# Kernel tuning notes

Hardware: AMD Instinct MI355X
Metric: run time of the kernel (lower is better)

The kernel has to match this reference:

```python
import jax, jax.numpy as jnp
import numpy as np

NEG_SLOPE = 0.2  # PyG GATConv default leaky_relu slope
EPS = 1e-16      # PyG softmax denominator epsilon


def gat_conv(x, src, dst, W, a_src, a_dst, num_nodes):
    """Single-head PyG GATConv (concat=True, heads=1, no bias), self-loops already in src/dst."""
    h = x @ W                                  # [N, out]
    alpha_src = h @ a_src                      # [N]
    alpha_dst = h @ a_dst                      # [N]
    e = jax.nn.leaky_relu(alpha_src[src] + alpha_dst[dst], NEG_SLOPE)  # [E]
    # segment softmax over destination nodes
    m = jax.ops.segment_max(e, dst, num_segments=num_nodes)           # [N]
    ex = jnp.exp(e - m[dst])                                          # [E]
    denom = jax.ops.segment_sum(ex, dst, num_segments=num_nodes)      # [N]
    alpha = ex / (denom[dst] + EPS)                                   # [E]
    # scatter-add weighted source features to destinations
    out = jax.ops.segment_sum(h[src] * alpha[:, None], dst, num_segments=num_nodes)
    return out


def setup_inputs() -> dict:
    key = jax.random.key(0)
    N, E, F_in, H, C = 100000, 1600000, 256, 64, 40
    ks = jax.random.split(key, 12)
    x = jax.random.normal(ks[0], (N, F_in), dtype=jnp.float32)
    edge_index = jax.random.randint(ks[1], (2, E), 0, N, dtype=jnp.int64)
    s = 0.1
    return {
        "x": x,
        "edge_index": edge_index,
        "W0": jax.random.normal(ks[2], (F_in, H), dtype=jnp.float32) * s,
        "asrc0": jax.random.normal(ks[3], (H,), dtype=jnp.float32) * s,
        "adst0": jax.random.normal(ks[4], (H,), dtype=jnp.float32) * s,
        "W1": jax.random.normal(ks[5], (H, H), dtype=jnp.float32) * s,
        "asrc1": jax.random.normal(ks[6], (H,), dtype=jnp.float32) * s,
        "adst1": jax.random.normal(ks[7], (H,), dtype=jnp.float32) * s,
        "W2": jax.random.normal(ks[8], (H, C), dtype=jnp.float32) * s,
        "asrc2": jax.random.normal(ks[9], (C,), dtype=jnp.float32) * s,
        "adst2": jax.random.normal(ks[10], (C,), dtype=jnp.float32) * s,
    }


def reference(x, edge_index, W0, asrc0, adst0, W1, asrc1, adst1, W2, asrc2, adst2):
    N = x.shape[0]
    # PyG GATConv add_self_loops=True: append (i, i) for every node
    loops = jnp.arange(N, dtype=edge_index.dtype)
    src = jnp.concatenate([edge_index[0], loops])
    dst = jnp.concatenate([edge_index[1], loops])
    params = [(W0, asrc0, adst0), (W1, asrc1, adst1), (W2, asrc2, adst2)]
    h = x
    for i, (W, a_s, a_d) in enumerate(params):
        h = gat_conv(h, src, dst, W, a_s, a_d, N)
        # type_norm='None' -> batch_norm is identity; eval mode -> no dropout/side losses
        if i != len(params) - 1:
            h = jax.nn.relu(h)
    return h
```

## Files before the change

### kernel.cpp

```cpp
#include <hip/hip_runtime.h>
#include <hip/hip_fp16.h>

#define CAP 56
#define BINW 128
#define CAPB 2560
#define CHUNK 4096
#define NEG_SLOPE 0.2f

__global__ void k_initcur(int* __restrict__ gcur, int nbin) {
    int i = blockIdx.x * blockDim.x + threadIdx.x;
    if (i < nbin) gcur[i] = i * CAPB;
}

__global__ __launch_bounds__(256) void k_bin(const int* __restrict__ esrc,
                                             const int* __restrict__ edst,
                                             int E, int N, int nbin,
                                             int* __restrict__ gcur,
                                             int* __restrict__ binbuf) {
    __shared__ int hist[1024];
    __shared__ int base[1024];

    const int tid = threadIdx.x;
    const int tot = E + N;
    const int start = blockIdx.x * CHUNK;
    const int end = (start + CHUNK < tot) ? start + CHUNK : tot;

    for (int i = tid; i < nbin; i += 256) hist[i] = 0;
    __syncthreads();

    for (int i = start + tid; i < end; i += 256) {
        int d = (i < E) ? edst[i] : (i - E);
        atomicAdd(&hist[d >> 7], 1);
    }
    __syncthreads();

    for (int i = tid; i < nbin; i += 256) {
        int h = hist[i];
        base[i] = h ? atomicAdd(&gcur[i], h) : 0;
    }
    __syncthreads();
    for (int i = tid; i < nbin; i += 256) hist[i] = 0;
    __syncthreads();

    for (int i = start + tid; i < end; i += 256) {
        int s, d;
        if (i < E) { s = esrc[i]; d = edst[i]; }
        else       { s = i - E;   d = s; }
        int b = d >> 7;
        int p = base[b] + atomicAdd(&hist[b], 1);
        if (p < (b + 1) * CAPB)
            binbuf[p] = ((d & (BINW - 1)) << 17) | s;
    }
}

__global__ __launch_bounds__(256) void k_bucket_bin(const int* __restrict__ binbuf,
                                                    const int* __restrict__ gcur,
                                                    int N,
                                                    int* __restrict__ cnt,
                                                    int* __restrict__ bucket) {
    __shared__ int lcnt[BINW];
    __shared__ int lb[BINW * CAP];

    const int tid = threadIdx.x;
    const int b = blockIdx.x;

    int n = gcur[b] - b * CAPB;
    if (n > CAPB) n = CAPB;

    for (int i = tid; i < BINW; i += 256) lcnt[i] = 0;
    for (int i = tid; i < BINW * CAP; i += 256) lb[i] = 0;
    __syncthreads();

    const int* src = binbuf + (size_t)b * CAPB;
    for (int i = tid; i < n; i += 256) {
        int x = src[i];
        int s = x & 0x1ffff;
        int dl = x >> 17;
        int p = atomicAdd(&lcnt[dl], 1);
        if (p < CAP) lb[dl * CAP + p] = s;
    }
    __syncthreads();

    size_t gbase = (size_t)b * BINW * CAP;
    for (int i = tid; i < BINW * CAP; i += 256)
        bucket[gbase + i] = lb[i];
    for (int i = tid; i < BINW; i += 256) {
        int v = b * BINW + i;
        if (v < N) cnt[v] = (lcnt[i] < CAP) ? lcnt[i] : CAP;
    }
}

template <int K, int FR>
__global__ __launch_bounds__(256) void k_gemm_tiled(const float* __restrict__ X,
                                                    const float* __restrict__ W,
                                                    const float* __restrict__ a_s,
                                                    const float* __restrict__ a_d,
                                                    __half* __restrict__ H16,
                                                    float* __restrict__ AS,
                                                    float* __restrict__ AD,
                                                    int N) {
    constexpr int BM = 128, BK = 32;
    constexpr int FP = 64;
    constexpr int XS = BK + 4;

    __shared__ float Xs[BM * XS];
    __shared__ float Ws[BK * FP];

    const int tid = threadIdx.x;
    const int tx = tid & 15, ty = tid >> 4;
    const int row0 = blockIdx.x * BM;

    float acc[8][4];
#pragma unroll
    for (int i = 0; i < 8; ++i)
#pragma unroll
        for (int j = 0; j < 4; ++j) acc[i][j] = 0.f;

    for (int k0 = 0; k0 < K; k0 += BK) {
#pragma unroll
        for (int i = 0; i < 4; ++i) {
            int idx = tid + 256 * i;
            int r = idx >> 3;
            int c4 = idx & 7;
            int gr = row0 + r;
            float4 v = make_float4(0.f, 0.f, 0.f, 0.f);
            if (gr < N) v = *reinterpret_cast<const float4*>(X + (size_t)gr * K + k0 + c4 * 4);
            *reinterpret_cast<float4*>(&Xs[r * XS + c4 * 4]) = v;
        }
        for (int i = tid; i < BK * FP; i += 256) {
            int r = i >> 6, c = i & 63;
            Ws[i] = (c < FR) ? W[(size_t)(k0 + r) * FR + c] : 0.f;
        }
        __syncthreads();

#pragma unroll
        for (int kq = 0; kq < BK; kq += 4) {
            float4 av[8];
#pragma unroll
            for (int i = 0; i < 8; ++i)
                av[i] = *reinterpret_cast<const float4*>(&Xs[(ty + (i << 4)) * XS + kq]);
#pragma unroll
            for (int kk = 0; kk < 4; ++kk) {
                float4 bwv = *reinterpret_cast<const float4*>(&Ws[(kq + kk) * FP + 4 * tx]);
#pragma unroll
                for (int i = 0; i < 8; ++i) {
                    float xs = (kk == 0) ? av[i].x : (kk == 1) ? av[i].y : (kk == 2) ? av[i].z : av[i].w;
                    acc[i][0] = fmaf(xs, bwv.x, acc[i][0]);
                    acc[i][1] = fmaf(xs, bwv.y, acc[i][1]);
                    acc[i][2] = fmaf(xs, bwv.z, acc[i][2]);
                    acc[i][3] = fmaf(xs, bwv.w, acc[i][3]);
                }
            }
        }
        __syncthreads();
    }

    float asv[4], adv[4];
#pragma unroll
    for (int j = 0; j < 4; ++j) {
        int col = 4 * tx + j;
        asv[j] = (col < FR) ? a_s[col] : 0.f;
        adv[j] = (col < FR) ? a_d[col] : 0.f;
    }

#pragma unroll
    for (int i = 0; i < 8; ++i) {
        int gr = row0 + ty + 16 * i;
        float rs = 0.f, rd = 0.f;
#pragma unroll
        for (int j = 0; j < 4; ++j) {
            rs = fmaf(acc[i][j], asv[j], rs);
            rd = fmaf(acc[i][j], adv[j], rd);
        }
#pragma unroll
        for (int off = 1; off < 16; off <<= 1) {
            rs += __shfl_xor(rs, off);
            rd += __shfl_xor(rd, off);
        }
        if (gr < N) {
            if (4 * tx < FR) {
                __half2 p0 = __floats2half2_rn(acc[i][0], acc[i][1]);
                __half2 p1 = __floats2half2_rn(acc[i][2], acc[i][3]);
                uint2 pk;
                pk.x = *reinterpret_cast<unsigned*>(&p0);
                pk.y = *reinterpret_cast<unsigned*>(&p1);
                *reinterpret_cast<uint2*>(&H16[(size_t)gr * FR + 4 * tx]) = pk;
            }
            if (tx == 0) { AS[gr] = rs; AD[gr] = rd; }
        }
    }
}

template <int F, bool RELU>
__global__ __launch_bounds__(256) void k_aggregate(const __half* __restrict__ H16,
                                                   const float* __restrict__ AS,
                                                   const float* __restrict__ AD,
                                                   const int* __restrict__ cnt,
                                                   const int* __restrict__ bucket,
                                                   float* __restrict__ OUT,
                                                   int N) {
    int wid  = (blockIdx.x * blockDim.x + threadIdx.x) >> 6;
    int lane = threadIdx.x & 63;
    if (wid >= N) return;
    int v = wid;

    int deg = cnt[v];

    int s = -1;
    if (lane < deg) s = bucket[(size_t)v * CAP + lane];

    float adv = AD[v];
    float ev  = -3.4e38f;
    if (s >= 0) {
        float t = AS[s] + adv;
        ev = (t > 0.f) ? t : NEG_SLOPE * t;
    }

    float m = ev;
#pragma unroll
    for (int off = 32; off; off >>= 1) m = fmaxf(m, __shfl_xor(m, off));

    float ex = (s >= 0) ? __expf(ev - m) : 0.f;

    float dsum = ex;
#pragma unroll
    for (int off = 32; off; off >>= 1) dsum += __shfl_xor(dsum, off);

    float inv = 1.f / (dsum + 1e-16f);

    float acc0 = 0.f, acc1 = 0.f, acc2 = 0.f, acc3 = 0.f;
    int e = 0;
    for (; e + 4 <= deg; e += 4) {
        int   s0 = __shfl(s, e),      s1 = __shfl(s, e + 1);
        int   s2 = __shfl(s, e + 2),  s3 = __shfl(s, e + 3);
        float a0 = __shfl(ex, e),     a1 = __shfl(ex, e + 1);
        float a2 = __shfl(ex, e + 2), a3 = __shfl(ex, e + 3);
        if (lane < F) {
            float h0 = __half2float(H16[(size_t)s0 * F + lane]);
            float h1 = __half2float(H16[(size_t)s1 * F + lane]);
            float h2 = __half2float(H16[(size_t)s2 * F + lane]);
            float h3 = __half2float(H16[(size_t)s3 * F + lane]);
            acc0 = fmaf(h0, a0, acc0);
            acc1 = fmaf(h1, a1, acc1);
            acc2 = fmaf(h2, a2, acc2);
            acc3 = fmaf(h3, a3, acc3);
        }
    }
    for (; e < deg; ++e) {
        int   se = __shfl(s, e);
        float al = __shfl(ex, e);
        if (lane < F) acc0 = fmaf(__half2float(H16[(size_t)se * F + lane]), al, acc0);
    }
    float acc = (acc0 + acc1) + (acc2 + acc3);
    acc *= inv;
    if (RELU) acc = fmaxf(acc, 0.f);
    if (lane < F) OUT[(size_t)v * F + lane] = acc;
}

extern "C" void kernel_launch(void* const* d_in, const int* in_sizes, int n_in,
                              void* d_out, int out_size, void* d_ws, size_t ws_size,
                              hipStream_t stream) {
    const float* x     = (const float*)d_in[0];
    const int*   ei    = (const int*)d_in[1];
    const float* W0    = (const float*)d_in[2];
    const float* asrc0 = (const float*)d_in[3];
    const float* adst0 = (const float*)d_in[4];
    const float* W1    = (const float*)d_in[5];
    const float* asrc1 = (const float*)d_in[6];
    const float* adst1 = (const float*)d_in[7];
    const float* W2    = (const float*)d_in[8];
    const float* asrc2 = (const float*)d_in[9];
    const float* adst2 = (const float*)d_in[10];

    const int F_IN = 256, H_DIM = 64;
    int N = in_sizes[0] / F_IN;
    int E = in_sizes[1] / 2;
    int nbin = (N + BINW - 1) / BINW;

    const int* esrc = ei;
    const int* edst = ei + E;

    char* w = (char*)d_ws;
    float*  agg    = (float*)w;  w += (size_t)N * H_DIM * 4;
    __half* h16    = (__half*)w; w += (size_t)N * H_DIM * 2;
    float*  AS     = (float*)w;  w += (size_t)N * 4;
    float*  AD     = (float*)w;  w += (size_t)N * 4;
    int*    cnt    = (int*)w;    w += (size_t)N * 4;
    int*    bucket = (int*)w;    w += (size_t)nbin * BINW * CAP * 4;
    int*    binbuf = (int*)w;    w += (size_t)nbin * CAPB * 4;
    int*    gcur   = (int*)w;    w += (size_t)nbin * 4;

    float* out = (float*)d_out;

    k_initcur<<<(nbin + 255) / 256, 256, 0, stream>>>(gcur, nbin);
    {
        int tot = E + N;
        int blocks = (tot + CHUNK - 1) / CHUNK;
        k_bin<<<blocks, 256, 0, stream>>>(esrc, edst, E, N, nbin, gcur, binbuf);
    }
    k_bucket_bin<<<nbin, 256, 0, stream>>>(binbuf, gcur, N, cnt, bucket);

    int gb = (N + 127) / 128;
    int ab = (N + 3) / 4;

    k_gemm_tiled<256, 64><<<gb, 256, 0, stream>>>(x, W0, asrc0, adst0, h16, AS, AD, N);
    k_aggregate<64, true><<<ab, 256, 0, stream>>>(h16, AS, AD, cnt, bucket, agg, N);

    k_gemm_tiled<64, 64><<<gb, 256, 0, stream>>>(agg, W1, asrc1, adst1, h16, AS, AD, N);
    k_aggregate<64, true><<<ab, 256, 0, stream>>>(h16, AS, AD, cnt, bucket, agg, N);

    k_gemm_tiled<64, 40><<<gb, 256, 0, stream>>>(agg, W2, asrc2, adst2, h16, AS, AD, N);
    k_aggregate<40, false><<<ab, 256, 0, stream>>>(h16, AS, AD, cnt, bucket, out, N);
}
```

Baseline: 498.3 us.

## Replace FP32 tiled GEMM with split-FP16 MFMA GEMM and LDS-staged stores

```diff
diff --git a/kernel.cpp b/kernel.cpp
--- a/kernel.cpp
+++ b/kernel.cpp
@@ -6,6 +6,9 @@
 #define CAPB 2560
 #define CHUNK 4096
 #define NEG_SLOPE 0.2f
+
+typedef _Float16 f16x8 __attribute__((ext_vector_type(8)));
+typedef float    f32x4 __attribute__((ext_vector_type(4)));
 
 __global__ void k_initcur(int* __restrict__ gcur, int nbin) {
     int i = blockIdx.x * blockDim.x + threadIdx.x;
@@ -91,102 +94,148 @@
 }
 
 template <int K, int FR>
-__global__ __launch_bounds__(256) void k_gemm_tiled(const float* __restrict__ X,
-                                                    const float* __restrict__ W,
-                                                    const float* __restrict__ a_s,
-                                                    const float* __restrict__ a_d,
-                                                    __half* __restrict__ H16,
-                                                    float* __restrict__ AS,
-                                                    float* __restrict__ AD,
-                                                    int N) {
-    constexpr int BM = 128, BK = 32;
-    constexpr int FP = 64;
-    constexpr int XS = BK + 4;
-
-    __shared__ float Xs[BM * XS];
-    __shared__ float Ws[BK * FP];
-
-    const int tid = threadIdx.x;
-    const int tx = tid & 15, ty = tid >> 4;
-    const int row0 = blockIdx.x * BM;
-
-    float acc[8][4];
-#pragma unroll
-    for (int i = 0; i < 8; ++i)
-#pragma unroll
-        for (int j = 0; j < 4; ++j) acc[i][j] = 0.f;
-
-    for (int k0 = 0; k0 < K; k0 += BK) {
-#pragma unroll
-        for (int i = 0; i < 4; ++i) {
-            int idx = tid + 256 * i;
-            int r = idx >> 3;
-            int c4 = idx & 7;
-            int gr = row0 + r;
-            float4 v = make_float4(0.f, 0.f, 0.f, 0.f);
-            if (gr < N) v = *reinterpret_cast<const float4*>(X + (size_t)gr * K + k0 + c4 * 4);
-            *reinterpret_cast<float4*>(&Xs[r * XS + c4 * 4]) = v;
-        }
-        for (int i = tid; i < BK * FP; i += 256) {
-            int r = i >> 6, c = i & 63;
-            Ws[i] = (c < FR) ? W[(size_t)(k0 + r) * FR + c] : 0.f;
-        }
-        __syncthreads();
-
-#pragma unroll
-        for (int kq = 0; kq < BK; kq += 4) {
-            float4 av[8];
-#pragma unroll
-            for (int i = 0; i < 8; ++i)
-                av[i] = *reinterpret_cast<const float4*>(&Xs[(ty + (i << 4)) * XS + kq]);
-#pragma unroll
-            for (int kk = 0; kk < 4; ++kk) {
-                float4 bwv = *reinterpret_cast<const float4*>(&Ws[(kq + kk) * FP + 4 * tx]);
-#pragma unroll
-                for (int i = 0; i < 8; ++i) {
-                    float xs = (kk == 0) ? av[i].x : (kk == 1) ? av[i].y : (kk == 2) ? av[i].z : av[i].w;
-                    acc[i][0] = fmaf(xs, bwv.x, acc[i][0]);
-                    acc[i][1] = fmaf(xs, bwv.y, acc[i][1]);
-                    acc[i][2] = fmaf(xs, bwv.z, acc[i][2]);
-                    acc[i][3] = fmaf(xs, bwv.w, acc[i][3]);
-                }
-            }
-        }
-        __syncthreads();
-    }
-
-    float asv[4], adv[4];
-#pragma unroll
-    for (int j = 0; j < 4; ++j) {
-        int col = 4 * tx + j;
-        asv[j] = (col < FR) ? a_s[col] : 0.f;
-        adv[j] = (col < FR) ? a_d[col] : 0.f;
-    }
-
-#pragma unroll
-    for (int i = 0; i < 8; ++i) {
-        int gr = row0 + ty + 16 * i;
-        float rs = 0.f, rd = 0.f;
-#pragma unroll
-        for (int j = 0; j < 4; ++j) {
-            rs = fmaf(acc[i][j], asv[j], rs);
-            rd = fmaf(acc[i][j], adv[j], rd);
+__global__ __launch_bounds__(256) void k_gemm_mfma(const float* __restrict__ X,
+                                                   const float* __restrict__ W,
+                                                   const float* __restrict__ a_s,
+                                                   const float* __restrict__ a_d,
+                                                   __half* __restrict__ H16,
+                                                   float* __restrict__ AS,
+                                                   float* __restrict__ AD,
+                                                   int N) {
+    constexpr int NSTEP = K / 32;
+    constexpr int G = K / 8;
+    constexpr int SCR = 72;
+
+    __shared__ _Float16 Wt[64 * K];
+    __shared__ _Float16 scr[4][32 * SCR];
+
+    const int tid  = threadIdx.x;
+    const int wid  = tid >> 6;
+    const int lane = tid & 63;
+    const int lrow = lane & 15;
+    const int g    = lane >> 4;
+    const int row0 = blockIdx.x * 128 + wid * 32;
+
+    for (int i = tid; i < K * 64; i += 256) {
+        int k = i >> 6, c = i & 63;
+        float w = (c < FR) ? W[(size_t)k * FR + c] : 0.f;
+        int gr = (k >> 3) ^ (c & (G - 1));
+        Wt[c * K + gr * 8 + (k & 7)] = (_Float16)w;
+    }
+    __syncthreads();
+
+    f32x4 acc[2][4];
+#pragma unroll
+    for (int rf = 0; rf < 2; ++rf)
+#pragma unroll
+        for (int cf = 0; cf < 4; ++cf) {
+            f32x4 z = {0.f, 0.f, 0.f, 0.f};
+            acc[rf][cf] = z;
+        }
+
+    int r0 = row0 + lrow;      if (r0 > N - 1) r0 = N - 1;
+    int r1 = row0 + 16 + lrow; if (r1 > N - 1) r1 = N - 1;
+    const float* xp0 = X + (size_t)r0 * K + g * 8;
+    const float* xp1 = X + (size_t)r1 * K + g * 8;
+
+#pragma unroll
+    for (int ks = 0; ks < NSTEP; ++ks) {
+        float4 a0  = *reinterpret_cast<const float4*>(xp0 + ks * 32);
+        float4 a0b = *reinterpret_cast<const float4*>(xp0 + ks * 32 + 4);
+        float4 a1  = *reinterpret_cast<const float4*>(xp1 + ks * 32);
+        float4 a1b = *reinterpret_cast<const float4*>(xp1 + ks * 32 + 4);
+
+        f16x8 b[4];
+#pragma unroll
+        for (int cf = 0; cf < 4; ++cf) {
+            int c = cf * 16 + lrow;
+            int t = ks * 4 + g;
+            b[cf] = *reinterpret_cast<const f16x8*>(
+                &Wt[c * K + ((t ^ (c & (G - 1))) << 3)]);
+        }
+
+        float fa0[8] = {a0.x, a0.y, a0.z, a0.w, a0b.x, a0b.y, a0b.z, a0b.w};
+        float fa1[8] = {a1.x, a1.y, a1.z, a1.w, a1b.x, a1b.y, a1b.z, a1b.w};
+        f16x8 h0, l0, h1, l1;
+#pragma unroll
+        for (int j = 0; j < 8; ++j) {
+            _Float16 hv0 = (_Float16)fa0[j];
+            h0[j] = hv0; l0[j] = (_Float16)(fa0[j] - (float)hv0);
+            _Float16 hv1 = (_Float16)fa1[j];
+            h1[j] = hv1; l1[j] = (_Float16)(fa1[j] - (float)hv1);
+        }
+
+#pragma unroll
+        for (int cf = 0; cf < 4; ++cf) {
+            acc[0][cf] = __builtin_amdgcn_mfma_f32_16x16x32_f16(h0, b[cf], acc[0][cf], 0, 0, 0);
+            acc[0][cf] = __builtin_amdgcn_mfma_f32_16x16x32_f16(l0, b[cf], acc[0][cf], 0, 0, 0);
+            acc[1][cf] = __builtin_amdgcn_mfma_f32_16x16x32_f16(h1, b[cf], acc[1][cf], 0, 0, 0);
+            acc[1][cf] = __builtin_amdgcn_mfma_f32_16x16x32_f16(l1, b[cf], acc[1][cf], 0, 0, 0);
+        }
+    }
+
+#pragma unroll
+    for (int rf = 0; rf < 2; ++rf) {
+        float ss[4] = {0.f, 0.f, 0.f, 0.f}, sd[4] = {0.f, 0.f, 0.f, 0.f};
+#pragma unroll
+        for (int cf = 0; cf < 4; ++cf) {
+            int c = cf * 16 + lrow;
+            float va = (c < FR) ? a_s[c] : 0.f;
+            float vd = (c < FR) ? a_d[c] : 0.f;
+#pragma unroll
+            for (int q = 0; q < 4; ++q) {
+                ss[q] = fmaf(acc[rf][cf][q], va, ss[q]);
+                sd[q] = fmaf(acc[rf][cf][q], vd, sd[q]);
+            }
         }
 #pragma unroll
         for (int off = 1; off < 16; off <<= 1) {
-            rs += __shfl_xor(rs, off);
-            rd += __shfl_xor(rd, off);
-        }
-        if (gr < N) {
-            if (4 * tx < FR) {
-                __half2 p0 = __floats2half2_rn(acc[i][0], acc[i][1]);
-                __half2 p1 = __floats2half2_rn(acc[i][2], acc[i][3]);
-                uint2 pk;
-                pk.x = *reinterpret_cast<unsigned*>(&p0);
-                pk.y = *reinterpret_cast<unsigned*>(&p1);
-                *reinterpret_cast<uint2*>(&H16[(size_t)gr * FR + 4 * tx]) = pk;
-            }
-            if (tx == 0) { AS[gr] = rs; AD[gr] = rd; }
+#pragma unroll
+            for (int q = 0; q < 4; ++q) {
+                ss[q] += __shfl_xor(ss[q], off);
+                sd[q] += __shfl_xor(sd[q], off);
+            }
+        }
+        if (lrow == 0) {
+#pragma unroll
+            for (int q = 0; q < 4; ++q) {
+                int r = row0 + rf * 16 + g * 4 + q;
+                if (r < N) { AS[r] = ss[q]; AD[r] = sd[q]; }
+            }
+        }
+    }
+
+#pragma unroll
+    for (int rf = 0; rf < 2; ++rf)
+#pragma unroll
+        for (int cf = 0; cf < 4; ++cf)
+#pragma unroll
+            for (int q = 0; q < 4; ++q)
+                scr[wid][(rf * 16 + g * 4 + q) * SCR + cf * 16 + lrow] =
+                    (_Float16)acc[rf][cf][q];
+    __syncthreads();
+
+    if (FR == 64) {
+        int sr = lane >> 1, half = lane & 1;
+        int grow = row0 + sr;
+        if (grow < N) {
+#pragma unroll
+            for (int q = 0; q < 4; ++q) {
+                f16x8 v = *reinterpret_cast<const f16x8*>(
+                    &scr[wid][sr * SCR + half * 32 + q * 8]);
+                *reinterpret_cast<f16x8*>(&H16[(size_t)grow * 64 + half * 32 + q * 8]) = v;
+            }
+        }
+    } else {
+        constexpr int CH = FR / 8;
+        for (int idx = lane; idx < 32 * CH; idx += 64) {
+            int sr = idx / CH, c8 = idx % CH;
+            int grow = row0 + sr;
+            if (grow < N) {
+                f16x8 v = *reinterpret_cast<const f16x8*>(
+                    &scr[wid][sr * SCR + c8 * 8]);
+                *reinterpret_cast<f16x8*>(&H16[(size_t)grow * FR + c8 * 8]) = v;
+            }
         }
     }
 }
@@ -303,12 +352,12 @@
     int gb = (N + 127) / 128;
     int ab = (N + 3) / 4;
 
-    k_gemm_tiled<256, 64><<<gb, 256, 0, stream>>>(x, W0, asrc0, adst0, h16, AS, AD, N);
+    k_gemm_mfma<256, 64><<<gb, 256, 0, stream>>>(x, W0, asrc0, adst0, h16, AS, AD, N);
     k_aggregate<64, true><<<ab, 256, 0, stream>>>(h16, AS, AD, cnt, bucket, agg, N);
 
-    k_gemm_tiled<64, 64><<<gb, 256, 0, stream>>>(agg, W1, asrc1, adst1, h16, AS, AD, N);
+    k_gemm_mfma<64, 64><<<gb, 256, 0, stream>>>(agg, W1, asrc1, adst1, h16, AS, AD, N);
     k_aggregate<64, true><<<ab, 256, 0, stream>>>(h16, AS, AD, cnt, bucket, agg, N);
 
-    k_gemm_tiled<64, 40><<<gb, 256, 0, stream>>>(agg, W2, asrc2, adst2, h16, AS, AD, N);
+    k_gemm_mfma<64, 40><<<gb, 256, 0, stream>>>(agg, W2, asrc2, adst2, h16, AS, AD, N);
     k_aggregate<40, false><<<ab, 256, 0, stream>>>(h16, AS, AD, cnt, bucket, out, N);
 }
```

Result: faster. 473.6 us (-5.0%).
